# Optimization experiments

Measured on AMD Instinct MI355X. Metric: run time of the kernel, lower is better.

## Reference

```python
import jax, jax.numpy as jnp
import numpy as np

B, S, D, H = 2, 2048, 4096, 32
HD = D // H  # 128
AL = 10     # adapter_len


def _make_freqs(seq_len, head_dim, theta=10000.0):
    inv = 1.0 / (theta ** (np.arange(0, head_dim, 2, dtype=np.float32) / head_dim))
    t = np.arange(seq_len, dtype=np.float32)
    f = np.outer(t, inv)  # [S, HD/2]
    return jnp.asarray(np.cos(f)), jnp.asarray(np.sin(f))


def setup_inputs() -> dict:
    key = jax.random.key(0)
    ks = jax.random.split(key, 8)
    scale = 1.0 / np.sqrt(D)
    cos, sin = _make_freqs(S, HD)
    mask = jnp.triu(jnp.full((1, 1, S, S), -1e9, dtype=jnp.float32), k=1)
    return {
        "x": jax.random.normal(ks[0], (B, S, D), jnp.float32),
        "cos": cos,
        "sin": sin,
        "mask": mask,
        "wq": jax.random.normal(ks[1], (D, D), jnp.float32) * scale,
        "wk": jax.random.normal(ks[2], (D, D), jnp.float32) * scale,
        "wv": jax.random.normal(ks[3], (D, D), jnp.float32) * scale,
        "wo": jax.random.normal(ks[4], (D, D), jnp.float32) * scale,
        "gate": jnp.zeros((1, H, 1, 1), jnp.float32) + 0.1,
        "adapter": jax.random.normal(ks[5], (1, AL, D), jnp.float32),
        "random_init": 0,
    }


def _rope(x, cos, sin):
    # x: [B, S, H, HD]; rotate interleaved even/odd pairs (view_as_complex semantics)
    b, s, h, d = x.shape
    xr = x.reshape(b, s, h, d // 2, 2)
    x0, x1 = xr[..., 0], xr[..., 1]
    c = cos[None, :, None, :]
    sn = sin[None, :, None, :]
    o0 = x0 * c - x1 * sn
    o1 = x0 * sn + x1 * c
    return jnp.stack([o0, o1], axis=-1).reshape(b, s, h, d)


def reference(x, cos, sin, mask, wq, wk, wv, wo, gate, adapter, random_init):
    b, s, _ = x.shape
    inv_sqrt = 1.0 / np.sqrt(HD)
    xq = (x @ wq).reshape(b, s, H, HD)
    xk = (x @ wk).reshape(b, s, H, HD)
    xv = (x @ wv).reshape(b, s, H, HD)
    xq = _rope(xq, cos, sin)
    xk = _rope(xk, cos, sin)
    # start_pos=0 prefill: cache slice == xk/xv
    q = xq.transpose(0, 2, 1, 3)  # [B,H,S,HD]
    k = xk.transpose(0, 2, 1, 3)
    v = xv.transpose(0, 2, 1, 3)

    ak = (adapter @ wk).reshape(1, AL, H, HD).transpose(0, 2, 1, 3)  # [1,H,AL,HD]
    av = (adapter @ wv).reshape(1, AL, H, HD).transpose(0, 2, 1, 3)

    scores = jnp.einsum("bhqd,bhkd->bhqk", q, k) * inv_sqrt + mask
    a_scores = jnp.einsum("bhqd,bhkd->bhqk", q, jnp.broadcast_to(ak, (b, H, AL, HD))) * inv_sqrt

    if not random_init:
        p = jax.nn.softmax(scores, axis=-1)
        out = jnp.einsum("bhqk,bhkd->bhqd", p, v)
        ap = gate * jax.nn.softmax(a_scores, axis=-1)
        out = out + jnp.einsum("bhqk,bhkd->bhqd", ap, jnp.broadcast_to(av, (b, H, AL, HD)))
    else:
        total = jnp.concatenate([a_scores, scores], axis=3)
        p = jax.nn.softmax(total, axis=-1)
        tv = jnp.concatenate([jnp.broadcast_to(av, (b, H, AL, HD)), v], axis=2)
        out = jnp.einsum("bhqk,bhkd->bhqd", p, tv)

    out = out.transpose(0, 2, 1, 3).reshape(b, s, D)
    return out @ wo
```

## Files before the change

kernel.cpp:

```cpp
#include <hip/hip_runtime.h>

typedef __bf16 bf16_t;
typedef __bf16 bf16x8 __attribute__((ext_vector_type(8)));
typedef __bf16 bf16x4 __attribute__((ext_vector_type(4)));
typedef float floatx4 __attribute__((ext_vector_type(4)));

#define D_MODEL 4096
#define SEQ 2048
#define BATCH 2
#define NH 32
#define HD 128
#define AL 10
#define MROWS (BATCH * SEQ)
#define N_QKV (3 * D_MODEL)

static __device__ __forceinline__ void gload_lds16(const void* g, void* l) {
  __builtin_amdgcn_global_load_lds((const __attribute__((address_space(1))) void*)g,
                                   (__attribute__((address_space(3))) void*)l, 16, 0, 0);
}

#define DPP_MAX_STEP(v, ctrl)                                                             \
  v = fmaxf(v, __int_as_float(__builtin_amdgcn_update_dpp(                                \
                 __float_as_int(v), __float_as_int(v), ctrl, 0xF, 0xF, false)))
static __device__ __forceinline__ float rowmax16(float v) {
  DPP_MAX_STEP(v, 0x128);
  DPP_MAX_STEP(v, 0x124);
  DPP_MAX_STEP(v, 0x122);
  DPP_MAX_STEP(v, 0x121);
  return v;
}

__global__ void convert_bf16_kernel(const float* __restrict__ src, bf16_t* __restrict__ dst) {
  size_t i = ((size_t)blockIdx.x * 256 + threadIdx.x) * 4;
  float4 v = *(const float4*)(src + i);
  bf16x4 o;
  o[0] = (bf16_t)v.x; o[1] = (bf16_t)v.y; o[2] = (bf16_t)v.z; o[3] = (bf16_t)v.w;
  *(bf16x4*)(dst + i) = o;
}

__global__ void transpose_conv_kernel(const float* __restrict__ src, bf16_t* __restrict__ dst) {
  __shared__ float tile[32][33];
  const int tx = threadIdx.x & 31;
  const int ty = threadIdx.x >> 5;
  const int c0 = blockIdx.x * 32;
  const int r0 = blockIdx.y * 32;
#pragma unroll
  for (int i = 0; i < 4; i++) {
    int r = ty + i * 8;
    tile[r][tx] = src[(size_t)(r0 + r) * D_MODEL + c0 + tx];
  }
  __syncthreads();
#pragma unroll
  for (int i = 0; i < 4; i++) {
    int r = ty + i * 8;
    dst[(size_t)(c0 + r) * D_MODEL + r0 + tx] = (bf16_t)tile[tx][r];
  }
}

__global__ void vt_kernel(const bf16_t* __restrict__ QKV, bf16_t* __restrict__ VT) {
  __shared__ bf16_t tile[32][33];
  const int tx = threadIdx.x & 31;
  const int ty = threadIdx.x >> 5;
  const int s0 = blockIdx.x * 32;
  const int c0 = blockIdx.y * 32;
  const int b = blockIdx.z;
  const bf16_t* src = QKV + (size_t)b * SEQ * N_QKV + 2 * D_MODEL;
#pragma unroll
  for (int i = 0; i < 4; i++) {
    int r = ty + i * 8;
    tile[r][tx] = src[(size_t)(s0 + r) * N_QKV + c0 + tx];
  }
  __syncthreads();
  bf16_t* dst = VT + (size_t)b * D_MODEL * SEQ;
#pragma unroll
  for (int i = 0; i < 4; i++) {
    int r = ty + i * 8;
    dst[(size_t)(c0 + r) * SEQ + s0 + tx] = tile[tx][r];
  }
}

template <typename OT>
__global__ __launch_bounds__(256) void gemm_bt_kernel(const bf16_t* __restrict__ A,
                                                      const bf16_t* __restrict__ Bt,
                                                      OT* __restrict__ C, int M, int N, int K) {
  __shared__ __align__(16) bf16_t As[128 * 32];
  __shared__ __align__(16) bf16_t Bs[128 * 32];
  const int tid = threadIdx.x;
  const int lane = tid & 63;
  const int wave = tid >> 6;
  const int quad = lane >> 4;
  const int l16 = lane & 15;
  const int m0 = blockIdx.y * 128;
  const int n0 = blockIdx.x * 128;
  const int wm = (wave >> 1) * 64;
  const int wn = (wave & 1) * 64;
  floatx4 acc[4][4] = {};
  for (int k0 = 0; k0 < K; k0 += 32) {
#pragma unroll
    for (int r = 0; r < 2; r++) {
      int c = r * 256 + tid;
      gload_lds16(A + (size_t)(m0 + (c >> 2)) * K + k0 + (c & 3) * 8, As + c * 8);
      gload_lds16(Bt + (size_t)(n0 + (c >> 2)) * K + k0 + (c & 3) * 8, Bs + c * 8);
    }
    __syncthreads();
    bf16x8 af[4], bfv[4];
#pragma unroll
    for (int i = 0; i < 4; i++)
      af[i] = *(const bf16x8*)(As + (wm + i * 16 + l16) * 32 + quad * 8);
#pragma unroll
    for (int j = 0; j < 4; j++)
      bfv[j] = *(const bf16x8*)(Bs + (wn + j * 16 + l16) * 32 + quad * 8);
#pragma unroll
    for (int i = 0; i < 4; i++)
#pragma unroll
      for (int j = 0; j < 4; j++)
        acc[i][j] = __builtin_amdgcn_mfma_f32_16x16x32_bf16(af[i], bfv[j], acc[i][j], 0, 0, 0);
    __syncthreads();
  }
#pragma unroll
  for (int i = 0; i < 4; i++)
#pragma unroll
    for (int j = 0; j < 4; j++) {
      int m = m0 + wm + i * 16 + quad * 4;
      int n = n0 + wn + j * 16 + l16;
#pragma unroll
      for (int r = 0; r < 4; r++) C[(size_t)(m + r) * N + n] = (OT)acc[i][j][r];
    }
}

__global__ void rope_kernel(bf16_t* __restrict__ QKV, const float* __restrict__ cosb,
                            const float* __restrict__ sinb) {
  int idx = blockIdx.x * 256 + threadIdx.x;
  int i = idx & 63;
  int h = (idx >> 6) & 31;
  int half = (idx >> 11) & 1;
  int row = idx >> 12;
  int s = row & (SEQ - 1);
  size_t off = (size_t)row * N_QKV + half * D_MODEL + h * HD + 2 * i;
  float c = cosb[s * 64 + i], sn = sinb[s * 64 + i];
  float x0 = (float)QKV[off], x1 = (float)QKV[off + 1];
  QKV[off] = (bf16_t)(x0 * c - x1 * sn);
  QKV[off + 1] = (bf16_t)(x0 * sn + x1 * c);
}

__global__ void zero_kernel(float* __restrict__ p, int n) {
  int i = blockIdx.x * 256 + threadIdx.x;
  if (i < n) p[i] = 0.f;
}

__global__ __launch_bounds__(256) void adapter_gemm_kernel(const float* __restrict__ adp,
                                                           const float* __restrict__ wk,
                                                           const float* __restrict__ wv,
                                                           float* __restrict__ ak,
                                                           float* __restrict__ av) {
  const float* W = blockIdx.y ? wv : wk;
  float* out = blockIdx.y ? av : ak;
  const int n = blockIdx.x * 256 + threadIdx.x;
  const int kb = blockIdx.z * 512;
  __shared__ float a_s[AL][512];
  for (int t = threadIdx.x; t < AL * 512; t += 256)
    a_s[t / 512][t % 512] = adp[(t / 512) * D_MODEL + kb + (t % 512)];
  __syncthreads();
  float accv[AL] = {};
  for (int kk = 0; kk < 512; kk++) {
    float w = W[(size_t)(kb + kk) * D_MODEL + n];
#pragma unroll
    for (int a = 0; a < AL; a++) accv[a] += a_s[a][kk] * w;
  }
#pragma unroll
  for (int a = 0; a < AL; a++) atomicAdd(&out[a * D_MODEL + n], accv[a]);
}

__global__ __launch_bounds__(256) void flash_kernel(const bf16_t* __restrict__ QKV,
                                                    const bf16_t* __restrict__ VT,
                                                    const float* __restrict__ akp,
                                                    const float* __restrict__ avp,
                                                    const float* __restrict__ gatep,
                                                    bf16_t* __restrict__ Out) {
  const int lane = threadIdx.x & 63;
  const int wave = threadIdx.x >> 6;
  const int quad = lane >> 4;
  const int l16 = lane & 15;
  const int q0 = (gridDim.y - 1 - blockIdx.y) * 32;
  const int bh = blockIdx.x * 4 + wave;
  const int b = bh >> 5;
  const int h = bh & 31;
  const size_t base = (size_t)b * SEQ * N_QKV;
  const int hoff = h * HD;
  const float scale = 0.08838834764831845f;
  __shared__ __align__(16) bf16_t Pl[4][2][16][32];

  const bf16_t* vtb = VT + (size_t)(b * D_MODEL + hoff) * SEQ;

  bf16x8 onesf;
#pragma unroll
  for (int j = 0; j < 8; j++) onesf[j] = (bf16_t)1.0f;

  bf16x8 qa[2][4];
#pragma unroll
  for (int mt = 0; mt < 2; mt++) {
    const bf16_t* qrow = QKV + base + (size_t)(q0 + mt * 16 + l16) * N_QKV + hoff + quad * 8;
#pragma unroll
    for (int c = 0; c < 4; c++) qa[mt][c] = *(const bf16x8*)(qrow + c * 32);
  }
  floatx4 acc[2][8] = {};
  float Mx[2][4], Ls[2][4];
#pragma unroll
  for (int mt = 0; mt < 2; mt++)
#pragma unroll
    for (int r = 0; r < 4; r++) { Mx[mt][r] = -1e30f; Ls[mt][r] = 0.f; }

  for (int j0 = 0; j0 <= q0; j0 += 32) {
    bf16x8 kf[2][4];
#pragma unroll
    for (int nt = 0; nt < 2; nt++) {
      const bf16_t* krow =
          QKV + base + (size_t)(j0 + nt * 16 + l16) * N_QKV + D_MODEL + hoff + quad * 8;
#pragma unroll
      for (int c = 0; c < 4; c++) kf[nt][c] = *(const bf16x8*)(krow + c * 32);
    }
    bf16x8 vf[8];
#pragma unroll
    for (int dt = 0; dt < 8; dt++)
      vf[dt] = *(const bf16x8*)(vtb + (size_t)(dt * 16 + l16) * SEQ + j0 + quad * 8);

    const bool diag = (j0 == q0);
#pragma unroll
    for (int mt = 0; mt < 2; mt++) {
      floatx4 s0 = {}, s1 = {};
#pragma unroll
      for (int c = 0; c < 4; c++) {
        s0 = __builtin_amdgcn_mfma_f32_16x16x32_bf16(qa[mt][c], kf[0][c], s0, 0, 0, 0);
        s1 = __builtin_amdgcn_mfma_f32_16x16x32_bf16(qa[mt][c], kf[1][c], s1, 0, 0, 0);
      }
      const int rowg = q0 + mt * 16 + quad * 4;
#pragma unroll
      for (int r = 0; r < 4; r++) {
        float v0 = s0[r] * scale;
        float v1 = s1[r] * scale;
        if (diag) {
          if (j0 + l16 > rowg + r) v0 = -1e30f;
          if (j0 + 16 + l16 > rowg + r) v1 = -1e30f;
        }
        float mx = rowmax16(fmaxf(v0, v1));
        float nm = fmaxf(Mx[mt][r], mx);
        float alpha = __expf(Mx[mt][r] - nm);
        Mx[mt][r] = nm;
        float p0 = __expf(v0 - nm);
        float p1 = __expf(v1 - nm);
        Ls[mt][r] *= alpha;
        Pl[wave][mt][quad * 4 + r][l16] = (bf16_t)p0;
        Pl[wave][mt][quad * 4 + r][l16 + 16] = (bf16_t)p1;
#pragma unroll
        for (int dt = 0; dt < 8; dt++) acc[mt][dt][r] *= alpha;
      }
    }
    __syncthreads();
#pragma unroll
    for (int mt = 0; mt < 2; mt++) {
      bf16x8 pf = *(const bf16x8*)(&Pl[wave][mt][l16][quad * 8]);
      floatx4 lz = {};
      lz = __builtin_amdgcn_mfma_f32_16x16x32_bf16(pf, onesf, lz, 0, 0, 0);
#pragma unroll
      for (int dt = 0; dt < 8; dt++)
        acc[mt][dt] = __builtin_amdgcn_mfma_f32_16x16x32_bf16(pf, vf[dt], acc[mt][dt], 0, 0, 0);
#pragma unroll
      for (int r = 0; r < 4; r++) Ls[mt][r] += lz[r];
    }
    __syncthreads();
  }

  const float gate = gatep[h];
#pragma unroll
  for (int mt = 0; mt < 2; mt++) {
    floatx4 sa = {};
#pragma unroll
    for (int c = 0; c < 4; c++) {
      bf16x8 bak;
#pragma unroll
      for (int jj = 0; jj < 8; jj++) {
        float v = (l16 < AL) ? akp[(size_t)l16 * D_MODEL + hoff + c * 32 + quad * 8 + jj] : 0.f;
        bak[jj] = (bf16_t)v;
      }
      sa = __builtin_amdgcn_mfma_f32_16x16x32_bf16(qa[mt][c], bak, sa, 0, 0, 0);
    }
#pragma unroll
    for (int r = 0; r < 4; r++) {
      float v = (l16 < AL) ? sa[r] * scale : -1e30f;
      float mx = rowmax16(v);
      float p = __expf(v - mx);
      float rs = p;
#pragma unroll
      for (int off = 8; off; off >>= 1) rs += __shfl_xor(rs, off, 64);
      float pa = p / rs;
      Pl[wave][mt][quad * 4 + r][l16] = (l16 < AL) ? (bf16_t)pa : (bf16_t)0.f;
      Pl[wave][mt][quad * 4 + r][l16 + 16] = (bf16_t)0.f;
    }
  }
  __syncthreads();
  bf16x8 avf[8];
#pragma unroll
  for (int jj = 0; jj < 8; jj++) {
    int j = quad * 8 + jj;
#pragma unroll
    for (int dt = 0; dt < 8; dt++) {
      float v = (j < AL) ? avp[(size_t)j * D_MODEL + hoff + dt * 16 + l16] : 0.f;
      avf[dt][jj] = (bf16_t)v;
    }
  }
#pragma unroll
  for (int mt = 0; mt < 2; mt++) {
    bf16x8 pf = *(const bf16x8*)(&Pl[wave][mt][l16][quad * 8]);
#pragma unroll
    for (int dt = 0; dt < 8; dt++) {
      floatx4 z = {};
      floatx4 oa = __builtin_amdgcn_mfma_f32_16x16x32_bf16(pf, avf[dt], z, 0, 0, 0);
#pragma unroll
      for (int r = 0; r < 4; r++) {
        int m = q0 + mt * 16 + quad * 4 + r;
        float val = acc[mt][dt][r] / Ls[mt][r] + gate * oa[r];
        Out[(size_t)(b * SEQ + m) * D_MODEL + hoff + dt * 16 + l16] = (bf16_t)val;
      }
    }
  }
}

extern "C" void kernel_launch(void* const* d_in, const int* in_sizes, int n_in, void* d_out,
                              int out_size, void* d_ws, size_t ws_size, hipStream_t stream) {
  const float* x = (const float*)d_in[0];
  const float* cosb = (const float*)d_in[1];
  const float* sinb = (const float*)d_in[2];
  const float* wq = (const float*)d_in[4];
  const float* wk = (const float*)d_in[5];
  const float* wv = (const float*)d_in[6];
  const float* wo = (const float*)d_in[7];
  const float* gate = (const float*)d_in[8];
  const float* adp = (const float*)d_in[9];
  float* out = (float*)d_out;

  char* ws = (char*)d_ws;
  const size_t DD = (size_t)D_MODEL * D_MODEL;
  bf16_t* Wt = (bf16_t*)(ws);
  bf16_t* Wot = (bf16_t*)(ws + 3 * DD * 2);
  bf16_t* Xb = (bf16_t*)(ws + 4 * DD * 2);
  bf16_t* QKV = (bf16_t*)(ws + 5 * DD * 2);
  bf16_t* Att = (bf16_t*)(ws + 8 * DD * 2);
  float* akb = (float*)(ws + 9 * DD * 2);
  float* avb = akb + AL * D_MODEL;
  bf16_t* VT = Xb;

  convert_bf16_kernel<<<MROWS * D_MODEL / 1024, 256, 0, stream>>>(x, Xb);
  transpose_conv_kernel<<<dim3(128, 128), 256, 0, stream>>>(wq, Wt);
  transpose_conv_kernel<<<dim3(128, 128), 256, 0, stream>>>(wk, Wt + DD);
  transpose_conv_kernel<<<dim3(128, 128), 256, 0, stream>>>(wv, Wt + 2 * DD);
  transpose_conv_kernel<<<dim3(128, 128), 256, 0, stream>>>(wo, Wot);
  gemm_bt_kernel<bf16_t><<<dim3(N_QKV / 128, MROWS / 128), 256, 0, stream>>>(
      Xb, Wt, QKV, MROWS, N_QKV, D_MODEL);
  rope_kernel<<<(MROWS * 4096) / 256, 256, 0, stream>>>(QKV, cosb, sinb);
  vt_kernel<<<dim3(SEQ / 32, D_MODEL / 32, BATCH), 256, 0, stream>>>(QKV, VT);
  zero_kernel<<<(2 * AL * D_MODEL + 255) / 256, 256, 0, stream>>>(akb, 2 * AL * D_MODEL);
  adapter_gemm_kernel<<<dim3(D_MODEL / 256, 2, 8), 256, 0, stream>>>(adp, wk, wv, akb, avb);
  flash_kernel<<<dim3((BATCH * NH) / 4, SEQ / 32), 256, 0, stream>>>(QKV, VT, akb, avb, gate,
                                                                     Att);
  gemm_bt_kernel<float><<<dim3(D_MODEL / 128, MROWS / 128), 256, 0, stream>>>(
      Att, Wot, out, MROWS, D_MODEL, D_MODEL);
}
```

Measured before the change: 1.602 ms.

## Replace GEMM with 256x256-tile, double-buffered, swizzled-LDS 8-wave kernel

The 128x128 single-buffered bf16 GEMM used for the QKV and output projections is replaced by a 512-thread kernel with 256x256 tiles and K-step 64. Global-to-LDS loads are double buffered two tiles ahead, with explicit vmcnt waits, and interleaved with MFMA phases under barriers and setprio. LDS chunks are XOR-swizzled to avoid bank conflicts, and the block index is remapped so neighbouring blocks share operands in cache. The goal is more data reuse per block and global load latency hidden behind matrix math. The cost is higher register and LDS use, about 128KB of LDS per block, which lowers occupancy.

```diff
diff --git a/kernel.cpp b/kernel.cpp
--- a/kernel.cpp
+++ b/kernel.cpp
@@ -79,52 +79,176 @@
   }
 }
 
+
+static __device__ __forceinline__ void stage_half(const bf16_t* src, int ld, int k0,
+                                                  bf16_t* dst, int tid) {
+#pragma unroll
+  for (int rr = 0; rr < 2; rr++) {
+    const int c = tid + rr * 512;
+    const int row = c >> 3;
+    const int j = (c & 7) ^ (row & 7);
+    gload_lds16(src + (size_t)row * ld + k0 + j * 8, dst + c * 8);
+  }
+}
+
+static __device__ __forceinline__ bf16x8 read_frag(const bf16_t* half, int row, int chunk) {
+  const int j = chunk ^ (row & 7);
+  return *(const bf16x8*)(half + row * 64 + j * 8);
+}
+
+#define GSBAR() __builtin_amdgcn_s_barrier()
+#define GSCHED0() __builtin_amdgcn_sched_barrier(0)
+#define WAIT_LGKM0() asm volatile("s_waitcnt lgkmcnt(0)" ::: "memory")
+#define WAIT_VM8() asm volatile("s_waitcnt vmcnt(8)" ::: "memory")
+#define WAIT_VM0() asm volatile("s_waitcnt vmcnt(0)" ::: "memory")
+
 template <typename OT>
-__global__ __launch_bounds__(256) void gemm_bt_kernel(const bf16_t* __restrict__ A,
+__global__ __launch_bounds__(512) void gemm256_kernel(const bf16_t* __restrict__ A,
                                                       const bf16_t* __restrict__ Bt,
                                                       OT* __restrict__ C, int M, int N, int K) {
-  __shared__ __align__(16) bf16_t As[128 * 32];
-  __shared__ __align__(16) bf16_t Bs[128 * 32];
+  __shared__ __align__(16) bf16_t sA[2][2][128 * 64];
+  __shared__ __align__(16) bf16_t sB[2][2][128 * 64];
   const int tid = threadIdx.x;
   const int lane = tid & 63;
   const int wave = tid >> 6;
+  const int wm = wave >> 2;
+  const int wn = wave & 3;
   const int quad = lane >> 4;
   const int l16 = lane & 15;
-  const int m0 = blockIdx.y * 128;
-  const int n0 = blockIdx.x * 128;
-  const int wm = (wave >> 1) * 64;
-  const int wn = (wave & 1) * 64;
-  floatx4 acc[4][4] = {};
-  for (int k0 = 0; k0 < K; k0 += 32) {
-#pragma unroll
-    for (int r = 0; r < 2; r++) {
-      int c = r * 256 + tid;
-      gload_lds16(A + (size_t)(m0 + (c >> 2)) * K + k0 + (c & 3) * 8, As + c * 8);
-      gload_lds16(Bt + (size_t)(n0 + (c >> 2)) * K + k0 + (c & 3) * 8, Bs + c * 8);
-    }
-    __syncthreads();
-    bf16x8 af[4], bfv[4];
-#pragma unroll
-    for (int i = 0; i < 4; i++)
-      af[i] = *(const bf16x8*)(As + (wm + i * 16 + l16) * 32 + quad * 8);
-#pragma unroll
-    for (int j = 0; j < 4; j++)
-      bfv[j] = *(const bf16x8*)(Bs + (wn + j * 16 + l16) * 32 + quad * 8);
-#pragma unroll
-    for (int i = 0; i < 4; i++)
-#pragma unroll
-      for (int j = 0; j < 4; j++)
-        acc[i][j] = __builtin_amdgcn_mfma_f32_16x16x32_bf16(af[i], bfv[j], acc[i][j], 0, 0, 0);
-    __syncthreads();
-  }
-#pragma unroll
-  for (int i = 0; i < 4; i++)
-#pragma unroll
-    for (int j = 0; j < 4; j++) {
-      int m = m0 + wm + i * 16 + quad * 4;
-      int n = n0 + wn + j * 16 + l16;
-#pragma unroll
-      for (int r = 0; r < 4; r++) C[(size_t)(m + r) * N + n] = (OT)acc[i][j][r];
+  const int nbx = gridDim.x;
+  const int nwg = nbx * gridDim.y;
+  const int lin = blockIdx.y * nbx + blockIdx.x;
+  const int cpx = nwg >> 3;
+  const int swz = (lin & 7) * cpx + (lin >> 3);
+  const int m0 = (swz / nbx) * 256;
+  const int n0 = (swz % nbx) * 256;
+  const int NT = K >> 6;
+  const int brow = (wn & 1) * 64;
+
+  floatx4 acc[8][4] = {};
+
+  stage_half(A + (size_t)m0 * K, K, 0, sA[0][0], tid);
+  stage_half(A + (size_t)(m0 + 128) * K, K, 0, sA[0][1], tid);
+  stage_half(Bt + (size_t)n0 * K, K, 0, sB[0][0], tid);
+  stage_half(Bt + (size_t)(n0 + 128) * K, K, 0, sB[0][1], tid);
+  stage_half(A + (size_t)m0 * K, K, 64, sA[1][0], tid);
+  stage_half(A + (size_t)(m0 + 128) * K, K, 64, sA[1][1], tid);
+  stage_half(Bt + (size_t)n0 * K, K, 64, sB[1][0], tid);
+  stage_half(Bt + (size_t)(n0 + 128) * K, K, 64, sB[1][1], tid);
+  WAIT_VM8();
+  GSCHED0();
+  GSBAR();
+
+  for (int t = 0; t < NT; t++) {
+    const int p = t & 1;
+    const bf16_t* Ah = sA[p][wm];
+    const bf16_t* Bh = sB[p][wn >> 1];
+    bf16x8 afr[4][2], bfr[4][2];
+
+#pragma unroll
+    for (int i = 0; i < 4; i++)
+#pragma unroll
+      for (int kk = 0; kk < 2; kk++) afr[i][kk] = read_frag(Ah, i * 16 + l16, kk * 4 + quad);
+#pragma unroll
+    for (int n = 0; n < 2; n++)
+#pragma unroll
+      for (int kk = 0; kk < 2; kk++)
+        bfr[n][kk] = read_frag(Bh, brow + n * 16 + l16, kk * 4 + quad);
+    GSBAR();
+    WAIT_LGKM0();
+    GSCHED0();
+    __builtin_amdgcn_s_setprio(1);
+#pragma unroll
+    for (int i = 0; i < 4; i++)
+#pragma unroll
+      for (int n = 0; n < 2; n++)
+#pragma unroll
+        for (int kk = 0; kk < 2; kk++)
+          acc[i][n] =
+              __builtin_amdgcn_mfma_f32_16x16x32_bf16(afr[i][kk], bfr[n][kk], acc[i][n], 0, 0, 0);
+    __builtin_amdgcn_s_setprio(0);
+    GSCHED0();
+    GSBAR();
+
+#pragma unroll
+    for (int n = 2; n < 4; n++)
+#pragma unroll
+      for (int kk = 0; kk < 2; kk++)
+        bfr[n][kk] = read_frag(Bh, brow + n * 16 + l16, kk * 4 + quad);
+    GSBAR();
+    WAIT_LGKM0();
+    GSCHED0();
+    __builtin_amdgcn_s_setprio(1);
+#pragma unroll
+    for (int i = 0; i < 4; i++)
+#pragma unroll
+      for (int n = 2; n < 4; n++)
+#pragma unroll
+        for (int kk = 0; kk < 2; kk++)
+          acc[i][n] =
+              __builtin_amdgcn_mfma_f32_16x16x32_bf16(afr[i][kk], bfr[n][kk], acc[i][n], 0, 0, 0);
+    __builtin_amdgcn_s_setprio(0);
+    GSCHED0();
+    GSBAR();
+
+#pragma unroll
+    for (int i = 0; i < 4; i++)
+#pragma unroll
+      for (int kk = 0; kk < 2; kk++)
+        afr[i][kk] = read_frag(Ah, (i + 4) * 16 + l16, kk * 4 + quad);
+    if (t + 2 < NT) {
+      const int k2 = (t + 2) << 6;
+      stage_half(Bt + (size_t)n0 * K, K, k2, sB[p][0], tid);
+      stage_half(Bt + (size_t)(n0 + 128) * K, K, k2, sB[p][1], tid);
+    }
+    GSBAR();
+    WAIT_LGKM0();
+    GSCHED0();
+    __builtin_amdgcn_s_setprio(1);
+#pragma unroll
+    for (int i = 0; i < 4; i++)
+#pragma unroll
+      for (int n = 0; n < 2; n++)
+#pragma unroll
+        for (int kk = 0; kk < 2; kk++)
+          acc[i + 4][n] = __builtin_amdgcn_mfma_f32_16x16x32_bf16(afr[i][kk], bfr[n][kk],
+                                                                  acc[i + 4][n], 0, 0, 0);
+    __builtin_amdgcn_s_setprio(0);
+    GSCHED0();
+    GSBAR();
+
+    if (t + 2 < NT) {
+      const int k2 = (t + 2) << 6;
+      stage_half(A + (size_t)m0 * K, K, k2, sA[p][0], tid);
+      stage_half(A + (size_t)(m0 + 128) * K, K, k2, sA[p][1], tid);
+      WAIT_VM8();
+    } else if (t + 1 < NT) {
+      WAIT_VM0();
+    }
+    GSCHED0();
+    GSBAR();
+    __builtin_amdgcn_s_setprio(1);
+#pragma unroll
+    for (int i = 0; i < 4; i++)
+#pragma unroll
+      for (int n = 2; n < 4; n++)
+#pragma unroll
+        for (int kk = 0; kk < 2; kk++)
+          acc[i + 4][n] = __builtin_amdgcn_mfma_f32_16x16x32_bf16(afr[i][kk], bfr[n][kk],
+                                                                  acc[i + 4][n], 0, 0, 0);
+    __builtin_amdgcn_s_setprio(0);
+    GSCHED0();
+    GSBAR();
+  }
+
+#pragma unroll
+  for (int i = 0; i < 8; i++)
+#pragma unroll
+    for (int n = 0; n < 4; n++) {
+      const int m = m0 + wm * 128 + i * 16 + quad * 4;
+      const int col = n0 + wn * 64 + n * 16 + l16;
+#pragma unroll
+      for (int r = 0; r < 4; r++) C[(size_t)(m + r) * N + col] = (OT)acc[i][n][r];
     }
 }
 
@@ -354,7 +478,7 @@
   transpose_conv_kernel<<<dim3(128, 128), 256, 0, stream>>>(wk, Wt + DD);
   transpose_conv_kernel<<<dim3(128, 128), 256, 0, stream>>>(wv, Wt + 2 * DD);
   transpose_conv_kernel<<<dim3(128, 128), 256, 0, stream>>>(wo, Wot);
-  gemm_bt_kernel<bf16_t><<<dim3(N_QKV / 128, MROWS / 128), 256, 0, stream>>>(
+  gemm256_kernel<bf16_t><<<dim3(N_QKV / 256, MROWS / 256), 512, 0, stream>>>(
       Xb, Wt, QKV, MROWS, N_QKV, D_MODEL);
   rope_kernel<<<(MROWS * 4096) / 256, 256, 0, stream>>>(QKV, cosb, sinb);
   vt_kernel<<<dim3(SEQ / 32, D_MODEL / 32, BATCH), 256, 0, stream>>>(QKV, VT);
@@ -362,6 +486,6 @@
   adapter_gemm_kernel<<<dim3(D_MODEL / 256, 2, 8), 256, 0, stream>>>(adp, wk, wv, akb, avb);
   flash_kernel<<<dim3((BATCH * NH) / 4, SEQ / 32), 256, 0, stream>>>(QKV, VT, akb, avb, gate,
                                                                      Att);
-  gemm_bt_kernel<float><<<dim3(D_MODEL / 128, MROWS / 128), 256, 0, stream>>>(
+  gemm256_kernel<float><<<dim3(D_MODEL / 256, MROWS / 256), 512, 0, stream>>>(
       Att, Wot, out, MROWS, D_MODEL, D_MODEL);
 }
```

New measurement: 1.448 ms. 1.11x faster.
